# Performance work log

Measured on AMD Instinct MI355X. Metric: run time of the kernel, lower is better.

## Reference

```python
import jax, jax.numpy as jnp
import numpy as np

N = 50000   # nodes
E = 800000  # edges
F = 256     # in_channels
H = 256     # hidden (GCN output)


def setup_inputs() -> dict:
    key = jax.random.key(0)
    ks = jax.random.split(key, 6)
    x = jax.random.normal(ks[0], (N, F), jnp.float32)
    edge_index = jax.random.randint(ks[1], (2, E), 0, N)
    perm = jax.random.permutation(ks[2], N)
    W = jax.random.normal(ks[3], (F, H), jnp.float32) / np.sqrt(F)
    b = jnp.zeros((H,), jnp.float32)
    a = jnp.full((1,), 0.25, jnp.float32)  # PReLU slope
    disc_W = jax.random.normal(ks[4], (H, H), jnp.float32) / np.sqrt(H)
    return {"x": x, "W": W, "b": b, "a": a, "disc_W": disc_W,
            "edge_index": edge_index, "perm": perm}


def _gcn(x, W, b, src, dst, n):
    # GCNConv: linear -> symmetric-normalized aggregation (with self-loops) -> bias
    xw = x @ W  # [N, H]
    loop = jnp.arange(n)
    s = jnp.concatenate([src, loop])
    d = jnp.concatenate([dst, loop])
    ew = jnp.ones(s.shape[0], xw.dtype)
    deg = jax.ops.segment_sum(ew, d, num_segments=n)          # [N]
    dinv = jnp.where(deg > 0, jax.lax.rsqrt(deg), 0.0)
    norm = dinv[s] * dinv[d]                                   # [E+N]
    out = jax.ops.segment_sum(xw[s] * norm[:, None], d, num_segments=n)
    return out + b


def reference(x, W, b, a, disc_W, edge_index, perm):
    src, dst = edge_index[0], edge_index[1]
    n = x.shape[0]

    def encode(feat):
        h = _gcn(feat, W, b, src, dst, n)
        return jnp.where(h >= 0, h, a * h)  # PReLU

    z1 = encode(x)          # clean
    z2 = encode(x[perm])    # corrupted (row permutation)
    summary = jax.nn.sigmoid(z1.mean(axis=0))  # [H]
    wsum = disc_W @ summary                     # [H]
    pos = z1 @ wsum  # [N]
    neg = z2 @ wsum  # [N]
    return pos, neg
```

## Files before the change

kernel.cpp:

```cpp
#include <hip/hip_runtime.h>

#define N_NODES 50000
#define N_EDGES 800000
#define DIM 256
#define NB 196
#define CSB 512

typedef __attribute__((ext_vector_type(8))) short bf16x8;
typedef __attribute__((ext_vector_type(4))) float f32x4;

__device__ __forceinline__ unsigned int f2bf(float f) {
  unsigned int u = __float_as_uint(f);
  return (u + 0x7FFFu + ((u >> 16) & 1u)) >> 16;
}
__device__ __forceinline__ float bf_lo(unsigned int u) {
  return __uint_as_float(u << 16);
}
__device__ __forceinline__ float bf_hi(unsigned int u) {
  return __uint_as_float(u & 0xFFFF0000u);
}


__global__ void k_deg(const int* __restrict__ dst, int* __restrict__ deg) {
  int e = blockIdx.x * blockDim.x + threadIdx.x;
  if (e < N_EDGES) atomicAdd(&deg[dst[e]], 1);
}

__global__ __launch_bounds__(256) void k_bsum(const int* __restrict__ deg,
                                              float* __restrict__ dinv,
                                              int* __restrict__ bsum) {
  __shared__ int red[4];
  const int t = threadIdx.x;
  const int i = blockIdx.x * 256 + t;
  int d = 0;
  if (i < N_NODES) {
    d = deg[i];
    dinv[i] = rsqrtf((float)(d + 1));
  }
  int s = d;
#pragma unroll
  for (int off = 32; off > 0; off >>= 1) s += __shfl_down(s, off);
  if ((t & 63) == 0) red[t >> 6] = s;
  __syncthreads();
  if (t == 0) bsum[blockIdx.x] = red[0] + red[1] + red[2] + red[3];
}

__global__ __launch_bounds__(256) void k_bscan(const int* __restrict__ bsum,
                                               int* __restrict__ boff,
                                               int* __restrict__ row_start) {
  __shared__ int s[256];
  const int t = threadIdx.x;
  int v = (t < NB) ? bsum[t] : 0;
  s[t] = v;
  __syncthreads();
  for (int off = 1; off < 256; off <<= 1) {
    int u = (t >= off) ? s[t - off] : 0;
    __syncthreads();
    s[t] += u;
    __syncthreads();
  }
  if (t < NB) boff[t] = s[t] - v;
  if (t == 0) row_start[N_NODES] = N_EDGES;
}

__global__ __launch_bounds__(256) void k_rowstart(const int* __restrict__ deg,
                                                  const int* __restrict__ boff,
                                                  int* __restrict__ row_start,
                                                  int* __restrict__ cursor) {
  __shared__ int s[256];
  const int t = threadIdx.x;
  const int i = blockIdx.x * 256 + t;
  int d = (i < N_NODES) ? deg[i] : 0;
  s[t] = d;
  __syncthreads();
  for (int off = 1; off < 256; off <<= 1) {
    int u = (t >= off) ? s[t - off] : 0;
    __syncthreads();
    s[t] += u;
    __syncthreads();
  }
  if (i < N_NODES) {
    int r = boff[blockIdx.x] + s[t] - d;
    row_start[i] = r;
    cursor[i] = r;
  }
}

__global__ void k_scatter(const int* __restrict__ src, const int* __restrict__ dst,
                          const int* __restrict__ perm, const float* __restrict__ dinv,
                          int* __restrict__ cursor, int* __restrict__ colidx,
                          int* __restrict__ colidx2, float* __restrict__ colnorm) {
  int e = blockIdx.x * blockDim.x + threadIdx.x;
  if (e < N_EDGES) {
    int s = src[e], d = dst[e];
    int p = atomicAdd(&cursor[d], 1);
    colidx[p] = s;
    colidx2[p] = perm[s];
    colnorm[p] = dinv[s] * dinv[d];
  }
}


__global__ void k_prep(const float* __restrict__ W, ushort* __restrict__ Wt) {
  int n = blockIdx.x, k = threadIdx.x;
  Wt[n * DIM + k] = (ushort)f2bf(W[k * DIM + n]);
}


__global__ __launch_bounds__(512) void k_gemm(const float* __restrict__ X,
                                              const ushort* __restrict__ Wt,
                                              ushort* __restrict__ XW) {
  __shared__ ushort Xs[128 * 40];
  __shared__ ushort Ws[256 * 40];
  const int tid = threadIdx.x;
  const int lane = tid & 63;
  const int w = tid >> 6;
  const int wm = w >> 2, wn = w & 3;
  const int m0 = blockIdx.x * 128;
  const int l16 = lane & 15, kh = lane >> 4;

  f32x4 acc[4][4];
#pragma unroll
  for (int mf = 0; mf < 4; ++mf)
#pragma unroll
    for (int nf = 0; nf < 4; ++nf) acc[mf][nf] = (f32x4){0.f, 0.f, 0.f, 0.f};

  for (int k0 = 0; k0 < DIM; k0 += 32) {
#pragma unroll
    for (int it = 0; it < 2; ++it) {
      int idx = tid + it * 512;
      int row = idx >> 3, q = idx & 7;
      int grow = m0 + row;
      float4 v = make_float4(0.f, 0.f, 0.f, 0.f);
      if (grow < N_NODES)
        v = *reinterpret_cast<const float4*>(&X[(size_t)grow * DIM + k0 + q * 4]);
      uint2 p;
      p.x = f2bf(v.x) | (f2bf(v.y) << 16);
      p.y = f2bf(v.z) | (f2bf(v.w) << 16);
      *reinterpret_cast<uint2*>(&Xs[row * 40 + q * 4]) = p;
    }
#pragma unroll
    for (int it = 0; it < 2; ++it) {
      int idx = tid + it * 512;
      int n = idx >> 2, c = idx & 3;
      uint4 wv = *reinterpret_cast<const uint4*>(&Wt[n * DIM + k0 + c * 8]);
      *reinterpret_cast<uint4*>(&Ws[n * 40 + c * 8]) = wv;
    }
    __syncthreads();
    bf16x8 a[4], b[4];
#pragma unroll
    for (int f = 0; f < 4; ++f) {
      a[f] = *reinterpret_cast<const bf16x8*>(&Ws[(wn * 64 + f * 16 + l16) * 40 + kh * 8]);
      b[f] = *reinterpret_cast<const bf16x8*>(&Xs[(wm * 64 + f * 16 + l16) * 40 + kh * 8]);
    }
#pragma unroll
    for (int mf = 0; mf < 4; ++mf)
#pragma unroll
      for (int nf = 0; nf < 4; ++nf)
        acc[mf][nf] = __builtin_amdgcn_mfma_f32_16x16x32_bf16(a[nf], b[mf],
                                                              acc[mf][nf], 0, 0, 0);
    __syncthreads();
  }
#pragma unroll
  for (int mf = 0; mf < 4; ++mf) {
    int m = m0 + wm * 64 + mf * 16 + l16;
    if (m >= N_NODES) continue;
#pragma unroll
    for (int nf = 0; nf < 4; ++nf) {
      int nb = wn * 64 + nf * 16 + kh * 4;
      uint2 p;
      p.x = f2bf(acc[mf][nf][0]) | (f2bf(acc[mf][nf][1]) << 16);
      p.y = f2bf(acc[mf][nf][2]) | (f2bf(acc[mf][nf][3]) << 16);
      *reinterpret_cast<uint2*>(&XW[(size_t)m * DIM + nb]) = p;
    }
  }
}


struct Acc8 { float a[8]; };

__device__ __forceinline__ void fma8(Acc8& A, uint4 v, float n) {
  A.a[0] = fmaf(bf_lo(v.x), n, A.a[0]);
  A.a[1] = fmaf(bf_hi(v.x), n, A.a[1]);
  A.a[2] = fmaf(bf_lo(v.y), n, A.a[2]);
  A.a[3] = fmaf(bf_hi(v.y), n, A.a[3]);
  A.a[4] = fmaf(bf_lo(v.z), n, A.a[4]);
  A.a[5] = fmaf(bf_hi(v.z), n, A.a[5]);
  A.a[6] = fmaf(bf_lo(v.w), n, A.a[6]);
  A.a[7] = fmaf(bf_hi(v.w), n, A.a[7]);
}

__device__ __forceinline__ void agg_loop2(const ushort* __restrict__ xw,
                                          const int* __restrict__ cidx,
                                          const float* __restrict__ cn,
                                          int e, int eEnd, int c, Acc8& A) {
  for (; e + 8 <= eEnd; e += 8) {
    int s[8]; float nn[8]; uint4 v[8];
#pragma unroll
    for (int j = 0; j < 8; ++j) { s[j] = cidx[e + j]; nn[j] = cn[e + j]; }
#pragma unroll
    for (int j = 0; j < 8; ++j)
      v[j] = *reinterpret_cast<const uint4*>(xw + (size_t)s[j] * DIM + c * 8);
#pragma unroll
    for (int j = 0; j < 8; ++j) fma8(A, v[j], nn[j]);
  }
  for (; e < eEnd; ++e) {
    uint4 v = *reinterpret_cast<const uint4*>(xw + (size_t)cidx[e] * DIM + c * 8);
    fma8(A, v, cn[e]);
  }
}

__device__ __forceinline__ void epilogue8(Acc8& A, const float* __restrict__ bias,
                                          float a0, int c) {
  float4 b0 = *reinterpret_cast<const float4*>(&bias[c * 8]);
  float4 b1 = *reinterpret_cast<const float4*>(&bias[c * 8 + 4]);
  A.a[0] += b0.x; A.a[1] += b0.y; A.a[2] += b0.z; A.a[3] += b0.w;
  A.a[4] += b1.x; A.a[5] += b1.y; A.a[6] += b1.z; A.a[7] += b1.w;
#pragma unroll
  for (int j = 0; j < 8; ++j) A.a[j] = A.a[j] >= 0.f ? A.a[j] : a0 * A.a[j];
}

__global__ __launch_bounds__(256) void k_agg1(
    const ushort* __restrict__ xw, const int* __restrict__ row_start,
    const int* __restrict__ colidx, const float* __restrict__ colnorm,
    const float* __restrict__ dinv, const float* __restrict__ bias,
    const float* __restrict__ slope, ushort* __restrict__ z1) {
  const int wid = (blockIdx.x * blockDim.x + threadIdx.x) >> 6;
  const int lane = threadIdx.x & 63;
  const int h = lane >> 5, c = lane & 31;
  const int r = wid * 2 + h;
  if (r >= N_NODES) return;
  const float di = dinv[r];
  Acc8 A;
#pragma unroll
  for (int j = 0; j < 8; ++j) A.a[j] = 0.f;
  uint4 sv = *reinterpret_cast<const uint4*>(xw + (size_t)r * DIM + c * 8);
  fma8(A, sv, di * di);
  agg_loop2(xw, colidx, colnorm, row_start[r], row_start[r + 1], c, A);
  epilogue8(A, bias, slope[0], c);
  uint4 p;
  p.x = f2bf(A.a[0]) | (f2bf(A.a[1]) << 16);
  p.y = f2bf(A.a[2]) | (f2bf(A.a[3]) << 16);
  p.z = f2bf(A.a[4]) | (f2bf(A.a[5]) << 16);
  p.w = f2bf(A.a[6]) | (f2bf(A.a[7]) << 16);
  *reinterpret_cast<uint4*>(z1 + (size_t)r * DIM + c * 8) = p;
}

__global__ __launch_bounds__(256) void k_agg2_neg(
    const ushort* __restrict__ xw, const int* __restrict__ row_start,
    const int* __restrict__ colidx2, const float* __restrict__ colnorm,
    const int* __restrict__ perm, const float* __restrict__ dinv,
    const float* __restrict__ bias, const float* __restrict__ slope,
    const float* __restrict__ wsum, float* __restrict__ neg) {
  const int wid = (blockIdx.x * blockDim.x + threadIdx.x) >> 6;
  const int lane = threadIdx.x & 63;
  const int h = lane >> 5, c = lane & 31;
  const int r = wid * 2 + h;
  if (r >= N_NODES) return;
  const float di = dinv[r];
  Acc8 A;
#pragma unroll
  for (int j = 0; j < 8; ++j) A.a[j] = 0.f;
  uint4 sv = *reinterpret_cast<const uint4*>(xw + (size_t)perm[r] * DIM + c * 8);
  fma8(A, sv, di * di);
  agg_loop2(xw, colidx2, colnorm, row_start[r], row_start[r + 1], c, A);
  epilogue8(A, bias, slope[0], c);
  float4 w0 = *reinterpret_cast<const float4*>(&wsum[c * 8]);
  float4 w1 = *reinterpret_cast<const float4*>(&wsum[c * 8 + 4]);
  float d = A.a[0] * w0.x + A.a[1] * w0.y + A.a[2] * w0.z + A.a[3] * w0.w +
            A.a[4] * w1.x + A.a[5] * w1.y + A.a[6] * w1.z + A.a[7] * w1.w;
#pragma unroll
  for (int off = 16; off > 0; off >>= 1) d += __shfl_down(d, off, 32);
  if (c == 0) neg[r] = d;
}


__global__ __launch_bounds__(256) void k_colsum(const ushort* __restrict__ z1,
                                                float* __restrict__ partial) {
  __shared__ float red[8 * 256];
  const int t = threadIdx.x;
  const int c8 = t & 31;
  const int g = t >> 5;
  float s[8] = {0.f, 0.f, 0.f, 0.f, 0.f, 0.f, 0.f, 0.f};
  for (int r = blockIdx.x * 8 + g; r < N_NODES; r += 8 * CSB) {
    uint4 v = *reinterpret_cast<const uint4*>(z1 + (size_t)r * DIM + c8 * 8);
    s[0] += bf_lo(v.x); s[1] += bf_hi(v.x);
    s[2] += bf_lo(v.y); s[3] += bf_hi(v.y);
    s[4] += bf_lo(v.z); s[5] += bf_hi(v.z);
    s[6] += bf_lo(v.w); s[7] += bf_hi(v.w);
  }
#pragma unroll
  for (int j = 0; j < 8; ++j) red[g * 256 + c8 * 8 + j] = s[j];
  __syncthreads();
  float tot = 0.f;
#pragma unroll
  for (int g2 = 0; g2 < 8; ++g2) tot += red[g2 * 256 + t];
  partial[blockIdx.x * 256 + t] = tot;
}

__global__ __launch_bounds__(256) void k_wsum(const float* __restrict__ partial,
                                              const float* __restrict__ disc_W,
                                              float* __restrict__ wsum) {
  __shared__ float s[DIM];
  const int t = threadIdx.x;
  float a0 = 0.f, a1 = 0.f, a2 = 0.f, a3 = 0.f;
  for (int b = 0; b < CSB; b += 4) {
    a0 += partial[(b + 0) * 256 + t];
    a1 += partial[(b + 1) * 256 + t];
    a2 += partial[(b + 2) * 256 + t];
    a3 += partial[(b + 3) * 256 + t];
  }
  float m = (a0 + a1 + a2 + a3) * (1.0f / (float)N_NODES);
  s[t] = 1.0f / (1.0f + expf(-m));
  __syncthreads();
  float acc = 0.f;
  for (int j = 0; j < DIM; j += 4) {
    float4 w4 = *reinterpret_cast<const float4*>(&disc_W[t * DIM + j]);
    acc += w4.x * s[j] + w4.y * s[j + 1] + w4.z * s[j + 2] + w4.w * s[j + 3];
  }
  wsum[t] = acc;
}

__global__ __launch_bounds__(256) void k_pos(const ushort* __restrict__ z1,
                                             const float* __restrict__ wsum,
                                             float* __restrict__ pos) {
  const int wid = (blockIdx.x * blockDim.x + threadIdx.x) >> 6;
  const int lane = threadIdx.x & 63;
  if (wid >= N_NODES) return;
  uint2 v = *reinterpret_cast<const uint2*>(z1 + (size_t)wid * DIM + lane * 4);
  float4 w4 = *reinterpret_cast<const float4*>(&wsum[lane * 4]);
  float d = bf_lo(v.x) * w4.x + bf_hi(v.x) * w4.y + bf_lo(v.y) * w4.z + bf_hi(v.y) * w4.w;
#pragma unroll
  for (int off = 32; off > 0; off >>= 1) d += __shfl_down(d, off);
  if (lane == 0) pos[wid] = d;
}


extern "C" void kernel_launch(void* const* d_in, const int* in_sizes, int n_in,
                              void* d_out, int out_size, void* d_ws, size_t ws_size,
                              hipStream_t stream) {
  const float* x      = (const float*)d_in[0];
  const float* W      = (const float*)d_in[1];
  const float* b      = (const float*)d_in[2];
  const float* a      = (const float*)d_in[3];
  const float* disc_W = (const float*)d_in[4];
  const int*   eidx   = (const int*)d_in[5];
  const int*   perm   = (const int*)d_in[6];
  const int* src = eidx;
  const int* dst = eidx + N_EDGES;

  constexpr size_t SZ_BFM  = (size_t)N_NODES * DIM * 2;
  constexpr size_t OFF_XW  = 0;
  constexpr size_t OFF_Z1  = OFF_XW + SZ_BFM;
  constexpr size_t OFF_WT  = OFF_Z1 + SZ_BFM;
  constexpr size_t OFF_DEG = OFF_WT + 131072;
  constexpr size_t OFF_DNV = OFF_DEG + 200192;
  constexpr size_t OFF_RS  = OFF_DNV + 200192;
  constexpr size_t OFF_CUR = OFF_RS + 200448;
  constexpr size_t OFF_CI  = OFF_CUR + 200192;
  constexpr size_t OFF_CI2 = OFF_CI + (size_t)N_EDGES * 4;
  constexpr size_t OFF_CN  = OFF_CI2 + (size_t)N_EDGES * 4;
  constexpr size_t OFF_WSM = OFF_CN + (size_t)N_EDGES * 4;
  constexpr size_t OFF_BS  = OFF_WSM + 1024;
  constexpr size_t OFF_BO  = OFF_BS + 1024;
  constexpr size_t OFF_PT  = OFF_BO + 1024;
  constexpr size_t NEED    = OFF_PT + (size_t)CSB * 256 * 4;
  if (ws_size < NEED) return;

  char* ws = (char*)d_ws;
  ushort* xw     = (ushort*)(ws + OFF_XW);
  ushort* z1     = (ushort*)(ws + OFF_Z1);
  ushort* Wt     = (ushort*)(ws + OFF_WT);
  int*    deg    = (int*)(ws + OFF_DEG);
  float*  dinv   = (float*)(ws + OFF_DNV);
  int*    rowst  = (int*)(ws + OFF_RS);
  int*    cursor = (int*)(ws + OFF_CUR);
  int*    colidx = (int*)(ws + OFF_CI);
  int*    colidx2= (int*)(ws + OFF_CI2);
  float*  colnorm= (float*)(ws + OFF_CN);
  float*  wsum   = (float*)(ws + OFF_WSM);
  int*    bsum   = (int*)(ws + OFF_BS);
  int*    boff   = (int*)(ws + OFF_BO);
  float*  partial= (float*)(ws + OFF_PT);

  float* pos = (float*)d_out;
  float* neg = pos + N_NODES;

  hipMemsetAsync(deg, 0, N_NODES * sizeof(int), stream);

  k_deg<<<(N_EDGES + 255) / 256, 256, 0, stream>>>(dst, deg);
  k_bsum<<<NB, 256, 0, stream>>>(deg, dinv, bsum);
  k_bscan<<<1, 256, 0, stream>>>(bsum, boff, rowst);
  k_rowstart<<<NB, 256, 0, stream>>>(deg, boff, rowst, cursor);
  k_scatter<<<(N_EDGES + 255) / 256, 256, 0, stream>>>(src, dst, perm, dinv,
                                                       cursor, colidx, colidx2, colnorm);

  k_prep<<<DIM, DIM, 0, stream>>>(W, Wt);
  k_gemm<<<(N_NODES + 127) / 128, 512, 0, stream>>>(x, Wt, xw);

  k_agg1<<<(N_NODES / 2 * 64) / 256, 256, 0, stream>>>(
      xw, rowst, colidx, colnorm, dinv, b, a, z1);
  k_colsum<<<CSB, 256, 0, stream>>>(z1, partial);
  k_wsum<<<1, 256, 0, stream>>>(partial, disc_W, wsum);

  k_pos<<<(N_NODES * 64 + 255) / 256, 256, 0, stream>>>(z1, wsum, pos);
  k_agg2_neg<<<(N_NODES / 2 * 64) / 256, 256, 0, stream>>>(
      xw, rowst, colidx2, colnorm, perm, dinv, b, a, wsum, neg);
}
```

Baseline: 278.3 us.

## Pad CSR rows to 16, pack edge metadata, fuse colsum and pos into aggregations

Each row's degree is rounded up to a multiple of 16. Zero-filled padding entries (index 0, norm 0) let the aggregation loop run fixed 16-wide batches with no tail loop, and edge index and norm are packed into one uint2 loaded cooperatively and broadcast with shuffles. The column sum is fused into k_agg1 through shared-memory reduction and atomics, the pos dot product is fused into the negative aggregation kernel, and wsum is spread over 32 blocks. In exchange the padding adds wasted gathers of row 0, there are extra memsets of the large metadata buffers, and float atomics make the summation order nondeterministic.

New measurement: 358.9 us. 29.0% more time.

```diff
diff --git a/kernel.cpp b/kernel.cpp
--- a/kernel.cpp
+++ b/kernel.cpp
@@ -4,7 +4,8 @@
 #define N_EDGES 800000
 #define DIM 256
 #define NB 196
-#define CSB 512
+#define UNROLL 16
+#define MAXE (N_EDGES + N_NODES * UNROLL)
 
 typedef __attribute__((ext_vector_type(8))) short bf16x8;
 typedef __attribute__((ext_vector_type(4))) float f32x4;
@@ -32,12 +33,13 @@
   __shared__ int red[4];
   const int t = threadIdx.x;
   const int i = blockIdx.x * 256 + t;
-  int d = 0;
+  int pd = 0;
   if (i < N_NODES) {
-    d = deg[i];
+    int d = deg[i];
     dinv[i] = rsqrtf((float)(d + 1));
-  }
-  int s = d;
+    pd = (d + UNROLL - 1) & ~(UNROLL - 1);
+  }
+  int s = pd;
 #pragma unroll
   for (int off = 32; off > 0; off >>= 1) s += __shfl_down(s, off);
   if ((t & 63) == 0) red[t >> 6] = s;
@@ -60,7 +62,7 @@
     __syncthreads();
   }
   if (t < NB) boff[t] = s[t] - v;
-  if (t == 0) row_start[N_NODES] = N_EDGES;
+  if (t == NB - 1) row_start[N_NODES] = s[NB - 1];
 }
 
 __global__ __launch_bounds__(256) void k_rowstart(const int* __restrict__ deg,
@@ -70,8 +72,8 @@
   __shared__ int s[256];
   const int t = threadIdx.x;
   const int i = blockIdx.x * 256 + t;
-  int d = (i < N_NODES) ? deg[i] : 0;
-  s[t] = d;
+  int pd = (i < N_NODES) ? ((deg[i] + UNROLL - 1) & ~(UNROLL - 1)) : 0;
+  s[t] = pd;
   __syncthreads();
   for (int off = 1; off < 256; off <<= 1) {
     int u = (t >= off) ? s[t - off] : 0;
@@ -80,7 +82,7 @@
     __syncthreads();
   }
   if (i < N_NODES) {
-    int r = boff[blockIdx.x] + s[t] - d;
+    int r = boff[blockIdx.x] + s[t] - pd;
     row_start[i] = r;
     cursor[i] = r;
   }
@@ -88,15 +90,15 @@
 
 __global__ void k_scatter(const int* __restrict__ src, const int* __restrict__ dst,
                           const int* __restrict__ perm, const float* __restrict__ dinv,
-                          int* __restrict__ cursor, int* __restrict__ colidx,
-                          int* __restrict__ colidx2, float* __restrict__ colnorm) {
+                          int* __restrict__ cursor, uint2* __restrict__ meta1,
+                          uint2* __restrict__ meta2) {
   int e = blockIdx.x * blockDim.x + threadIdx.x;
   if (e < N_EDGES) {
     int s = src[e], d = dst[e];
     int p = atomicAdd(&cursor[d], 1);
-    colidx[p] = s;
-    colidx2[p] = perm[s];
-    colnorm[p] = dinv[s] * dinv[d];
+    unsigned int nrm = __float_as_uint(dinv[s] * dinv[d]);
+    meta1[p] = make_uint2((unsigned)s, nrm);
+    meta2[p] = make_uint2((unsigned)perm[s], nrm);
   }
 }
 
@@ -190,23 +192,23 @@
   A.a[7] = fmaf(bf_hi(v.w), n, A.a[7]);
 }
 
-__device__ __forceinline__ void agg_loop2(const ushort* __restrict__ xw,
-                                          const int* __restrict__ cidx,
-                                          const float* __restrict__ cn,
-                                          int e, int eEnd, int c, Acc8& A) {
-  for (; e + 8 <= eEnd; e += 8) {
-    int s[8]; float nn[8]; uint4 v[8];
-#pragma unroll
-    for (int j = 0; j < 8; ++j) { s[j] = cidx[e + j]; nn[j] = cn[e + j]; }
-#pragma unroll
-    for (int j = 0; j < 8; ++j)
-      v[j] = *reinterpret_cast<const uint4*>(xw + (size_t)s[j] * DIM + c * 8);
-#pragma unroll
-    for (int j = 0; j < 8; ++j) fma8(A, v[j], nn[j]);
-  }
-  for (; e < eEnd; ++e) {
-    uint4 v = *reinterpret_cast<const uint4*>(xw + (size_t)cidx[e] * DIM + c * 8);
-    fma8(A, v, cn[e]);
+__device__ __forceinline__ void agg_ell(const ushort* __restrict__ xw,
+                                        const uint2* __restrict__ meta,
+                                        int e0, int e1, int c, Acc8& A) {
+  for (int e = e0; e < e1; e += UNROLL) {
+    uint2 mw = meta[e + (c & 15)];
+    int sj[UNROLL]; float nj[UNROLL];
+#pragma unroll
+    for (int j = 0; j < UNROLL; ++j) {
+      sj[j] = __shfl((int)mw.x, j, 32);
+      nj[j] = __uint_as_float(__shfl((int)mw.y, j, 32));
+    }
+    uint4 v[UNROLL];
+#pragma unroll
+    for (int j = 0; j < UNROLL; ++j)
+      v[j] = *reinterpret_cast<const uint4*>(xw + (size_t)sj[j] * DIM + c * 8);
+#pragma unroll
+    for (int j = 0; j < UNROLL; ++j) fma8(A, v[j], nj[j]);
   }
 }
 
@@ -222,21 +224,21 @@
 
 __global__ __launch_bounds__(256) void k_agg1(
     const ushort* __restrict__ xw, const int* __restrict__ row_start,
-    const int* __restrict__ colidx, const float* __restrict__ colnorm,
-    const float* __restrict__ dinv, const float* __restrict__ bias,
-    const float* __restrict__ slope, ushort* __restrict__ z1) {
-  const int wid = (blockIdx.x * blockDim.x + threadIdx.x) >> 6;
-  const int lane = threadIdx.x & 63;
+    const uint2* __restrict__ meta1, const float* __restrict__ dinv,
+    const float* __restrict__ bias, const float* __restrict__ slope,
+    ushort* __restrict__ z1, float* __restrict__ colsum) {
+  __shared__ float cred[8][256];
+  const int tid = threadIdx.x;
+  const int lane = tid & 63;
   const int h = lane >> 5, c = lane & 31;
-  const int r = wid * 2 + h;
-  if (r >= N_NODES) return;
+  const int r = ((blockIdx.x * 256 + tid) >> 6) * 2 + h;
   const float di = dinv[r];
   Acc8 A;
 #pragma unroll
   for (int j = 0; j < 8; ++j) A.a[j] = 0.f;
   uint4 sv = *reinterpret_cast<const uint4*>(xw + (size_t)r * DIM + c * 8);
   fma8(A, sv, di * di);
-  agg_loop2(xw, colidx, colnorm, row_start[r], row_start[r + 1], c, A);
+  agg_ell(xw, meta1, row_start[r], row_start[r + 1], c, A);
   epilogue8(A, bias, slope[0], c);
   uint4 p;
   p.x = f2bf(A.a[0]) | (f2bf(A.a[1]) << 16);
@@ -244,95 +246,70 @@
   p.z = f2bf(A.a[4]) | (f2bf(A.a[5]) << 16);
   p.w = f2bf(A.a[6]) | (f2bf(A.a[7]) << 16);
   *reinterpret_cast<uint4*>(z1 + (size_t)r * DIM + c * 8) = p;
-}
-
-__global__ __launch_bounds__(256) void k_agg2_neg(
-    const ushort* __restrict__ xw, const int* __restrict__ row_start,
-    const int* __restrict__ colidx2, const float* __restrict__ colnorm,
+  const int g = tid >> 5;
+#pragma unroll
+  for (int j = 0; j < 8; ++j) cred[g][c * 8 + j] = A.a[j];
+  __syncthreads();
+  float tot = 0.f;
+#pragma unroll
+  for (int g2 = 0; g2 < 8; ++g2) tot += cred[g2][tid];
+  unsafeAtomicAdd(&colsum[tid], tot);
+}
+
+__global__ __launch_bounds__(256) void k_agg2_negpos(
+    const ushort* __restrict__ xw, const ushort* __restrict__ z1,
+    const int* __restrict__ row_start, const uint2* __restrict__ meta2,
     const int* __restrict__ perm, const float* __restrict__ dinv,
     const float* __restrict__ bias, const float* __restrict__ slope,
-    const float* __restrict__ wsum, float* __restrict__ neg) {
-  const int wid = (blockIdx.x * blockDim.x + threadIdx.x) >> 6;
-  const int lane = threadIdx.x & 63;
+    const float* __restrict__ wsum, float* __restrict__ pos,
+    float* __restrict__ neg) {
+  const int tid = threadIdx.x;
+  const int lane = tid & 63;
   const int h = lane >> 5, c = lane & 31;
-  const int r = wid * 2 + h;
-  if (r >= N_NODES) return;
+  const int r = ((blockIdx.x * 256 + tid) >> 6) * 2 + h;
   const float di = dinv[r];
   Acc8 A;
 #pragma unroll
   for (int j = 0; j < 8; ++j) A.a[j] = 0.f;
   uint4 sv = *reinterpret_cast<const uint4*>(xw + (size_t)perm[r] * DIM + c * 8);
   fma8(A, sv, di * di);
-  agg_loop2(xw, colidx2, colnorm, row_start[r], row_start[r + 1], c, A);
+  agg_ell(xw, meta2, row_start[r], row_start[r + 1], c, A);
   epilogue8(A, bias, slope[0], c);
   float4 w0 = *reinterpret_cast<const float4*>(&wsum[c * 8]);
   float4 w1 = *reinterpret_cast<const float4*>(&wsum[c * 8 + 4]);
-  float d = A.a[0] * w0.x + A.a[1] * w0.y + A.a[2] * w0.z + A.a[3] * w0.w +
-            A.a[4] * w1.x + A.a[5] * w1.y + A.a[6] * w1.z + A.a[7] * w1.w;
-#pragma unroll
-  for (int off = 16; off > 0; off >>= 1) d += __shfl_down(d, off, 32);
-  if (c == 0) neg[r] = d;
-}
-
-
-__global__ __launch_bounds__(256) void k_colsum(const ushort* __restrict__ z1,
-                                                float* __restrict__ partial) {
-  __shared__ float red[8 * 256];
-  const int t = threadIdx.x;
-  const int c8 = t & 31;
-  const int g = t >> 5;
-  float s[8] = {0.f, 0.f, 0.f, 0.f, 0.f, 0.f, 0.f, 0.f};
-  for (int r = blockIdx.x * 8 + g; r < N_NODES; r += 8 * CSB) {
-    uint4 v = *reinterpret_cast<const uint4*>(z1 + (size_t)r * DIM + c8 * 8);
-    s[0] += bf_lo(v.x); s[1] += bf_hi(v.x);
-    s[2] += bf_lo(v.y); s[3] += bf_hi(v.y);
-    s[4] += bf_lo(v.z); s[5] += bf_hi(v.z);
-    s[6] += bf_lo(v.w); s[7] += bf_hi(v.w);
-  }
-#pragma unroll
-  for (int j = 0; j < 8; ++j) red[g * 256 + c8 * 8 + j] = s[j];
-  __syncthreads();
-  float tot = 0.f;
-#pragma unroll
-  for (int g2 = 0; g2 < 8; ++g2) tot += red[g2 * 256 + t];
-  partial[blockIdx.x * 256 + t] = tot;
-}
-
-__global__ __launch_bounds__(256) void k_wsum(const float* __restrict__ partial,
+  float dn = A.a[0] * w0.x + A.a[1] * w0.y + A.a[2] * w0.z + A.a[3] * w0.w +
+             A.a[4] * w1.x + A.a[5] * w1.y + A.a[6] * w1.z + A.a[7] * w1.w;
+  uint4 zv = *reinterpret_cast<const uint4*>(z1 + (size_t)r * DIM + c * 8);
+  float dp = bf_lo(zv.x) * w0.x + bf_hi(zv.x) * w0.y +
+             bf_lo(zv.y) * w0.z + bf_hi(zv.y) * w0.w +
+             bf_lo(zv.z) * w1.x + bf_hi(zv.z) * w1.y +
+             bf_lo(zv.w) * w1.z + bf_hi(zv.w) * w1.w;
+#pragma unroll
+  for (int off = 16; off > 0; off >>= 1) {
+    dn += __shfl_down(dn, off, 32);
+    dp += __shfl_down(dp, off, 32);
+  }
+  if (c == 0) { neg[r] = dn; pos[r] = dp; }
+}
+
+
+__global__ __launch_bounds__(256) void k_wsum(const float* __restrict__ colsum,
                                               const float* __restrict__ disc_W,
                                               float* __restrict__ wsum) {
   __shared__ float s[DIM];
   const int t = threadIdx.x;
-  float a0 = 0.f, a1 = 0.f, a2 = 0.f, a3 = 0.f;
-  for (int b = 0; b < CSB; b += 4) {
-    a0 += partial[(b + 0) * 256 + t];
-    a1 += partial[(b + 1) * 256 + t];
-    a2 += partial[(b + 2) * 256 + t];
-    a3 += partial[(b + 3) * 256 + t];
-  }
-  float m = (a0 + a1 + a2 + a3) * (1.0f / (float)N_NODES);
-  s[t] = 1.0f / (1.0f + expf(-m));
-  __syncthreads();
-  float acc = 0.f;
-  for (int j = 0; j < DIM; j += 4) {
-    float4 w4 = *reinterpret_cast<const float4*>(&disc_W[t * DIM + j]);
-    acc += w4.x * s[j] + w4.y * s[j + 1] + w4.z * s[j + 2] + w4.w * s[j + 3];
-  }
-  wsum[t] = acc;
-}
-
-__global__ __launch_bounds__(256) void k_pos(const ushort* __restrict__ z1,
-                                             const float* __restrict__ wsum,
-                                             float* __restrict__ pos) {
-  const int wid = (blockIdx.x * blockDim.x + threadIdx.x) >> 6;
-  const int lane = threadIdx.x & 63;
-  if (wid >= N_NODES) return;
-  uint2 v = *reinterpret_cast<const uint2*>(z1 + (size_t)wid * DIM + lane * 4);
-  float4 w4 = *reinterpret_cast<const float4*>(&wsum[lane * 4]);
-  float d = bf_lo(v.x) * w4.x + bf_hi(v.x) * w4.y + bf_lo(v.y) * w4.z + bf_hi(v.y) * w4.w;
-#pragma unroll
-  for (int off = 32; off > 0; off >>= 1) d += __shfl_down(d, off);
-  if (lane == 0) pos[wid] = d;
+  s[t] = 1.0f / (1.0f + expf(-colsum[t] * (1.0f / (float)N_NODES)));
+  __syncthreads();
+  const int g = t >> 5, c = t & 31;
+  const int o = blockIdx.x * 8 + g;
+  float4 w0 = *reinterpret_cast<const float4*>(&disc_W[o * DIM + c * 8]);
+  float4 w1 = *reinterpret_cast<const float4*>(&disc_W[o * DIM + c * 8 + 4]);
+  float acc = w0.x * s[c * 8] + w0.y * s[c * 8 + 1] + w0.z * s[c * 8 + 2] +
+              w0.w * s[c * 8 + 3] + w1.x * s[c * 8 + 4] + w1.y * s[c * 8 + 5] +
+              w1.z * s[c * 8 + 6] + w1.w * s[c * 8 + 7];
+#pragma unroll
+  for (int off = 16; off > 0; off >>= 1) acc += __shfl_down(acc, off, 32);
+  if (c == 0) wsum[o] = acc;
 }
 
 
@@ -350,6 +327,7 @@
   const int* dst = eidx + N_EDGES;
 
   constexpr size_t SZ_BFM  = (size_t)N_NODES * DIM * 2;
+  constexpr size_t SZ_META = (size_t)MAXE * 8;
   constexpr size_t OFF_XW  = 0;
   constexpr size_t OFF_Z1  = OFF_XW + SZ_BFM;
   constexpr size_t OFF_WT  = OFF_Z1 + SZ_BFM;
@@ -357,14 +335,13 @@
   constexpr size_t OFF_DNV = OFF_DEG + 200192;
   constexpr size_t OFF_RS  = OFF_DNV + 200192;
   constexpr size_t OFF_CUR = OFF_RS + 200448;
-  constexpr size_t OFF_CI  = OFF_CUR + 200192;
-  constexpr size_t OFF_CI2 = OFF_CI + (size_t)N_EDGES * 4;
-  constexpr size_t OFF_CN  = OFF_CI2 + (size_t)N_EDGES * 4;
-  constexpr size_t OFF_WSM = OFF_CN + (size_t)N_EDGES * 4;
+  constexpr size_t OFF_M1  = OFF_CUR + 200192;
+  constexpr size_t OFF_M2  = OFF_M1 + SZ_META;
+  constexpr size_t OFF_CS  = OFF_M2 + SZ_META;
+  constexpr size_t OFF_WSM = OFF_CS + 1024;
   constexpr size_t OFF_BS  = OFF_WSM + 1024;
   constexpr size_t OFF_BO  = OFF_BS + 1024;
-  constexpr size_t OFF_PT  = OFF_BO + 1024;
-  constexpr size_t NEED    = OFF_PT + (size_t)CSB * 256 * 4;
+  constexpr size_t NEED    = OFF_BO + 1024;
   if (ws_size < NEED) return;
 
   char* ws = (char*)d_ws;
@@ -375,35 +352,33 @@
   float*  dinv   = (float*)(ws + OFF_DNV);
   int*    rowst  = (int*)(ws + OFF_RS);
   int*    cursor = (int*)(ws + OFF_CUR);
-  int*    colidx = (int*)(ws + OFF_CI);
-  int*    colidx2= (int*)(ws + OFF_CI2);
-  float*  colnorm= (float*)(ws + OFF_CN);
+  uint2*  meta1  = (uint2*)(ws + OFF_M1);
+  uint2*  meta2  = (uint2*)(ws + OFF_M2);
+  float*  colsum = (float*)(ws + OFF_CS);
   float*  wsum   = (float*)(ws + OFF_WSM);
   int*    bsum   = (int*)(ws + OFF_BS);
   int*    boff   = (int*)(ws + OFF_BO);
-  float*  partial= (float*)(ws + OFF_PT);
 
   float* pos = (float*)d_out;
   float* neg = pos + N_NODES;
 
   hipMemsetAsync(deg, 0, N_NODES * sizeof(int), stream);
+  hipMemsetAsync(colsum, 0, DIM * sizeof(float), stream);
+  hipMemsetAsync(meta1, 0, SZ_META, stream);
+  hipMemsetAsync(meta2, 0, SZ_META, stream);
 
   k_deg<<<(N_EDGES + 255) / 256, 256, 0, stream>>>(dst, deg);
   k_bsum<<<NB, 256, 0, stream>>>(deg, dinv, bsum);
   k_bscan<<<1, 256, 0, stream>>>(bsum, boff, rowst);
   k_rowstart<<<NB, 256, 0, stream>>>(deg, boff, rowst, cursor);
   k_scatter<<<(N_EDGES + 255) / 256, 256, 0, stream>>>(src, dst, perm, dinv,
-                                                       cursor, colidx, colidx2, colnorm);
+                                                       cursor, meta1, meta2);
 
   k_prep<<<DIM, DIM, 0, stream>>>(W, Wt);
   k_gemm<<<(N_NODES + 127) / 128, 512, 0, stream>>>(x, Wt, xw);
 
-  k_agg1<<<(N_NODES / 2 * 64) / 256, 256, 0, stream>>>(
-      xw, rowst, colidx, colnorm, dinv, b, a, z1);
-  k_colsum<<<CSB, 256, 0, stream>>>(z1, partial);
-  k_wsum<<<1, 256, 0, stream>>>(partial, disc_W, wsum);
-
-  k_pos<<<(N_NODES * 64 + 255) / 256, 256, 0, stream>>>(z1, wsum, pos);
-  k_agg2_neg<<<(N_NODES / 2 * 64) / 256, 256, 0, stream>>>(
-      xw, rowst, colidx2, colnorm, perm, dinv, b, a, wsum, neg);
-}
+  k_agg1<<<N_NODES / 8, 256, 0, stream>>>(xw, rowst, meta1, dinv, b, a, z1, colsum);
+  k_wsum<<<32, 256, 0, stream>>>(colsum, disc_W, wsum);
+  k_agg2_negpos<<<N_NODES / 8, 256, 0, stream>>>(xw, z1, rowst, meta2, perm,
+                                                 dinv, b, a, wsum, pos, neg);
+}
```
